# Performance work log

Measured on AMD Instinct MI355X. Metric: run time of the kernel, lower is better.

## Reference

```python
import jax, jax.numpy as jnp
import numpy as np
from functools import partial

K = 64
KERNEL_SIZE = 16
TAU = 10.0
THETA = 0.5
GAMMA = 10.0
ALPHA = float(np.exp(-1.0 / TAU))
BETA = 1.0 - ALPHA

@jax.custom_vjp
def spike(x):
    return (x >= 0).astype(x.dtype)

def _spike_fwd(x):
    return spike(x), x

def _spike_bwd(x, g):
    surrogate = GAMMA * jnp.maximum(1.0 - GAMMA * jnp.abs(x), 0.0)
    return (g * surrogate,)

spike.defvjp(_spike_fwd, _spike_bwd)

def setup_inputs() -> dict:
    key = jax.random.key(0)
    k1, k2 = jax.random.split(key)
    B, T = 256, 4096
    x = jax.random.normal(k1, (B, 1, T), dtype=jnp.float32)
    # conv weight [K, 1, ks], init N(0, 1/sqrt(ks))
    W = jax.random.normal(k2, (K, 1, KERNEL_SIZE), dtype=jnp.float32) / np.sqrt(KERNEL_SIZE)
    return {"x": x, "W": W}

def _forward(x, W):
    B = x.shape[0]
    x = x.reshape(B, 1, -1)  # [B,1,T]
    # causal conv: left pad ks-1 -> output length T
    u = jax.lax.conv_general_dilated(
        x, W,
        window_strides=(1,),
        padding=[(KERNEL_SIZE - 1, 0)],
        dimension_numbers=("NCH", "OIH", "NCH"),
    )  # [B,K,T]
    u_t = jnp.transpose(u, (2, 0, 1))  # [T,B,K]
    v0 = jnp.zeros((B, K), dtype=x.dtype)

    def step(v, ut):
        v = ALPHA * v + BETA * ut                      # leak + input
        s_raw = spike(v - THETA)                        # [B,K]
        winner = jax.lax.stop_gradient(jnp.argmax(v, axis=1))  # [B]
        winner_spiked = jnp.take_along_axis(s_raw, winner[:, None], axis=1)  # [B,1]
        wta_mask = jax.nn.one_hot(winner, K, dtype=s_raw.dtype) * winner_spiked
        s = s_raw * wta_mask
        v = v - s * THETA                               # reset
        return v, s

    _, spikes_t = jax.lax.scan(step, v0, u_t)  # [T,B,K]
    return jnp.transpose(spikes_t, (1, 2, 0))  # [B,K,T]

def reference(x, W):
    return _forward(x, W)
```

## Files before the change

kernel.cpp:

```cpp
#include <hip/hip_runtime.h>

#define T_LEN  4096
#define KS     16
#define NSEG   8
#define SEG_CH 32
#define WARM_CH 20
#define USTRIDE 18

#define ALPHA_F 0.9048374180359595f
#define BETA_F  0.09516258196404048f
#define THETA_F 0.5f

__device__ __forceinline__ void barrier_lds() {
  asm volatile("s_waitcnt lgkmcnt(0)\n\ts_barrier" ::: "memory");
}

__device__ __forceinline__ float wave64_max_all(float v) {
  float m, t;
  asm("s_nop 1\n\t"
      "v_max_f32 %0, %2, %2 quad_perm:[1,0,3,2] row_mask:0xf bank_mask:0xf\n\t"
      "s_nop 1\n\t"
      "v_max_f32 %0, %0, %0 quad_perm:[2,3,0,1] row_mask:0xf bank_mask:0xf\n\t"
      "s_nop 1\n\t"
      "v_max_f32 %0, %0, %0 row_half_mirror row_mask:0xf bank_mask:0xf\n\t"
      "s_nop 1\n\t"
      "v_max_f32 %0, %0, %0 row_mirror row_mask:0xf bank_mask:0xf\n\t"
      "v_mov_b32 %1, %0\n\t"
      "s_nop 1\n\t"
      "v_permlane32_swap_b32 %1, %0\n\t"
      "s_nop 1\n\t"
      "v_max_f32 %0, %0, %1\n\t"
      "v_mov_b32 %1, %0\n\t"
      "s_nop 1\n\t"
      "v_permlane16_swap_b32 %1, %0\n\t"
      "s_nop 1\n\t"
      "v_max_f32 %0, %0, %1"
      : "=&v"(m), "=&v"(t)
      : "v"(v));
  return m;
}

__global__ __launch_bounds__(128, 4)
void convlif_wta_kernel(const float* __restrict__ x, const float* __restrict__ W,
                        float* __restrict__ out) {
  const int blk  = blockIdx.x;
  const int b    = blk >> 3;
  const int seg  = blk & (NSEG - 1);
  const int wave = threadIdx.x >> 6;
  const int lane = threadIdx.x & 63;

  const int cout0  = seg * SEG_CH;
  const int cstart = (cout0 > WARM_CH) ? (cout0 - WARM_CH) : 0;
  const int cend   = cout0 + SEG_CH;
  const int wpairs = (cout0 - cstart) >> 1;
  const int npair  = (cend - cstart) >> 1;

  __shared__ float dbuf[2][2][64][USTRIDE];

  const float4* xv4 = reinterpret_cast<const float4*>(x + (size_t)b * T_LEN);
  float* orow = out + ((size_t)(b * 64 + lane)) * T_LEN;

  if (wave == 1) {
    float w[KS];
    {
      const float4* w4 = reinterpret_cast<const float4*>(W + lane * KS);
      #pragma unroll
      for (int q = 0; q < 4; ++q) {
        float4 a = w4[q];
        w[4*q+0] = a.x; w[4*q+1] = a.y; w[4*q+2] = a.z; w[4*q+3] = a.w;
      }
    }

    for (int p = 0; p < npair; ++p) {
      #pragma unroll
      for (int ch = 0; ch < 2; ++ch) {
        const int c = cstart + 2 * p + ch;
        float xf[32];
        if (c == 0) {
          #pragma unroll
          for (int m = 0; m < 16; ++m) xf[m] = 0.0f;
        } else {
          const int b4 = 4 * c - 4;
          #pragma unroll
          for (int q = 0; q < 4; ++q) {
            float4 a = xv4[b4 + q];
            xf[4*q+0] = a.x; xf[4*q+1] = a.y; xf[4*q+2] = a.z; xf[4*q+3] = a.w;
          }
        }
        #pragma unroll
        for (int q = 0; q < 4; ++q) {
          float4 a = xv4[4*c + q];
          xf[16+4*q+0] = a.x; xf[16+4*q+1] = a.y;
          xf[16+4*q+2] = a.z; xf[16+4*q+3] = a.w;
        }

        float* ur = &dbuf[p & 1][ch][lane][0];
        #pragma unroll
        for (int i = 0; i < 16; i += 2) {
          float acc0 = w[0] * xf[1 + i];
          #pragma unroll
          for (int j = 1; j < KS; ++j) acc0 = fmaf(w[j], xf[1 + i + j], acc0);
          float acc1 = w[0] * xf[2 + i];
          #pragma unroll
          for (int j = 1; j < KS; ++j) acc1 = fmaf(w[j], xf[2 + i + j], acc1);
          *reinterpret_cast<float2*>(ur + i) =
              make_float2(BETA_F * acc0, BETA_F * acc1);
        }
      }
      barrier_lds();
    }
    barrier_lds();
  } else {
    float v = 0.0f;

    barrier_lds();

    for (int q = 0; q < wpairs; ++q) {
      const int slot = q & 1;
      #pragma unroll
      for (int ch = 0; ch < 2; ++ch) {
        float u[16];
        {
          const float* ur = &dbuf[slot][ch][lane][0];
          #pragma unroll
          for (int i = 0; i < 16; i += 2) {
            float2 t2 = *reinterpret_cast<const float2*>(ur + i);
            u[i] = t2.x; u[i + 1] = t2.y;
          }
        }
        #pragma unroll
        for (int i = 0; i < 16; ++i) {
          float vr = fmaf(ALPHA_F, v, u[i]);
          float vm = vr - THETA_F;
          unsigned long long sp = __ballot(vr >= THETA_F);
          bool c1 = (vr >= THETA_F);
          v = c1 ? vm : vr;
          if (__builtin_expect((sp & (sp - 1ull)) != 0ull, 0)) {
            float m = wave64_max_all(vr);
            unsigned long long eq = __ballot(vr == m);
            bool win = (lane == __builtin_ctzll(eq));
            v = win ? vm : vr;
          }
        }
      }
      barrier_lds();
    }

    for (int q = wpairs; q < npair; ++q) {
      const int slot = q & 1;
      #pragma unroll
      for (int ch = 0; ch < 2; ++ch) {
        const int c = cstart + 2 * q + ch;
        float u[16];
        {
          const float* ur = &dbuf[slot][ch][lane][0];
          #pragma unroll
          for (int i = 0; i < 16; i += 2) {
            float2 t2 = *reinterpret_cast<const float2*>(ur + i);
            u[i] = t2.x; u[i + 1] = t2.y;
          }
        }
        float sv[16];
        #pragma unroll
        for (int i = 0; i < 16; ++i) {
          float vr = fmaf(ALPHA_F, v, u[i]);
          float vm = vr - THETA_F;
          unsigned long long sp = __ballot(vr >= THETA_F);
          bool c1 = (vr >= THETA_F);
          sv[i] = c1 ? 1.0f : 0.0f;
          v     = c1 ? vm : vr;
          if (__builtin_expect((sp & (sp - 1ull)) != 0ull, 0)) {
            float m = wave64_max_all(vr);
            unsigned long long eq = __ballot(vr == m);
            bool win = (lane == __builtin_ctzll(eq));
            sv[i] = win ? 1.0f : 0.0f;
            v     = win ? vm : vr;
          }
        }
        float4* pp = reinterpret_cast<float4*>(orow + (size_t)c * 16);
        pp[0] = make_float4(sv[0],  sv[1],  sv[2],  sv[3]);
        pp[1] = make_float4(sv[4],  sv[5],  sv[6],  sv[7]);
        pp[2] = make_float4(sv[8],  sv[9],  sv[10], sv[11]);
        pp[3] = make_float4(sv[12], sv[13], sv[14], sv[15]);
      }
      barrier_lds();
    }
  }
}

extern "C" void kernel_launch(void* const* d_in, const int* in_sizes, int n_in,
                              void* d_out, int out_size, void* d_ws, size_t ws_size,
                              hipStream_t stream) {
  const float* x   = (const float*)d_in[0];
  const float* W   = (const float*)d_in[1];
  float*       out = (float*)d_out;
  convlif_wta_kernel<<<dim3(256 * NSEG), dim3(128), 0, stream>>>(x, W, out);
}
```

Before: 105.9 us.

## Split conv work between producer and consumer waves to balance load

The producer wave now computes the first 16 timesteps of the first chunk and only 8 of the second chunk in each pair. The consumer wave loads x directly and computes the remaining 8 conv outputs itself, before running the scan. This is meant to cut the producer's per-pair conv time, which gates the barrier pipeline, by moving part of its work onto the scan wave. In exchange the consumer wave takes extra global loads and FMAs, and every wave now loads the weights.

```diff
diff --git a/kernel.cpp b/kernel.cpp
--- a/kernel.cpp
+++ b/kernel.cpp
@@ -60,27 +60,28 @@
   const float4* xv4 = reinterpret_cast<const float4*>(x + (size_t)b * T_LEN);
   float* orow = out + ((size_t)(b * 64 + lane)) * T_LEN;
 
+  float w[KS];
+  {
+    const float4* w4 = reinterpret_cast<const float4*>(W + lane * KS);
+    #pragma unroll
+    for (int q = 0; q < 4; ++q) {
+      float4 a = w4[q];
+      w[4*q+0] = a.x; w[4*q+1] = a.y; w[4*q+2] = a.z; w[4*q+3] = a.w;
+    }
+  }
+
   if (wave == 1) {
-    float w[KS];
-    {
-      const float4* w4 = reinterpret_cast<const float4*>(W + lane * KS);
-      #pragma unroll
-      for (int q = 0; q < 4; ++q) {
-        float4 a = w4[q];
-        w[4*q+0] = a.x; w[4*q+1] = a.y; w[4*q+2] = a.z; w[4*q+3] = a.w;
-      }
-    }
-
     for (int p = 0; p < npair; ++p) {
-      #pragma unroll
-      for (int ch = 0; ch < 2; ++ch) {
-        const int c = cstart + 2 * p + ch;
+      const int c0 = cstart + 2 * p;
+      const int c1 = c0 + 1;
+
+      {
         float xf[32];
-        if (c == 0) {
+        if (c0 == 0) {
           #pragma unroll
           for (int m = 0; m < 16; ++m) xf[m] = 0.0f;
         } else {
-          const int b4 = 4 * c - 4;
+          const int b4 = 4 * c0 - 4;
           #pragma unroll
           for (int q = 0; q < 4; ++q) {
             float4 a = xv4[b4 + q];
@@ -89,14 +90,35 @@
         }
         #pragma unroll
         for (int q = 0; q < 4; ++q) {
-          float4 a = xv4[4*c + q];
+          float4 a = xv4[4*c0 + q];
           xf[16+4*q+0] = a.x; xf[16+4*q+1] = a.y;
           xf[16+4*q+2] = a.z; xf[16+4*q+3] = a.w;
         }
-
-        float* ur = &dbuf[p & 1][ch][lane][0];
+        float* ur = &dbuf[p & 1][0][lane][0];
         #pragma unroll
         for (int i = 0; i < 16; i += 2) {
+          float acc0 = w[0] * xf[1 + i];
+          #pragma unroll
+          for (int j = 1; j < KS; ++j) acc0 = fmaf(w[j], xf[1 + i + j], acc0);
+          float acc1 = w[0] * xf[2 + i];
+          #pragma unroll
+          for (int j = 1; j < KS; ++j) acc1 = fmaf(w[j], xf[2 + i + j], acc1);
+          *reinterpret_cast<float2*>(ur + i) =
+              make_float2(BETA_F * acc0, BETA_F * acc1);
+        }
+      }
+
+      {
+        float xf[24];
+        const int b4 = 4 * c1 - 4;
+        #pragma unroll
+        for (int q = 0; q < 6; ++q) {
+          float4 a = xv4[b4 + q];
+          xf[4*q+0] = a.x; xf[4*q+1] = a.y; xf[4*q+2] = a.z; xf[4*q+3] = a.w;
+        }
+        float* ur = &dbuf[p & 1][1][lane][0];
+        #pragma unroll
+        for (int i = 0; i < 8; i += 2) {
           float acc0 = w[0] * xf[1 + i];
           #pragma unroll
           for (int j = 1; j < KS; ++j) acc0 = fmaf(w[j], xf[1 + i + j], acc0);
@@ -112,63 +134,59 @@
     barrier_lds();
   } else {
     float v = 0.0f;
-
     barrier_lds();
 
-    for (int q = 0; q < wpairs; ++q) {
+    for (int q = 0; q < npair; ++q) {
       const int slot = q & 1;
+      const int c0 = cstart + 2 * q;
+      const int c1 = c0 + 1;
+      const bool outp = (q >= wpairs);
+
+      float u0[16], u1lo[8];
+      {
+        const float* ur0 = &dbuf[slot][0][lane][0];
+        #pragma unroll
+        for (int i = 0; i < 16; i += 2) {
+          float2 t2 = *reinterpret_cast<const float2*>(ur0 + i);
+          u0[i] = t2.x; u0[i + 1] = t2.y;
+        }
+        const float* ur1 = &dbuf[slot][1][lane][0];
+        #pragma unroll
+        for (int i = 0; i < 8; i += 2) {
+          float2 t2 = *reinterpret_cast<const float2*>(ur1 + i);
+          u1lo[i] = t2.x; u1lo[i + 1] = t2.y;
+        }
+      }
+
+      float xh[24];
+      {
+        const int bq = 4 * c1 - 2;
+        #pragma unroll
+        for (int qq = 0; qq < 6; ++qq) {
+          float4 a = xv4[bq + qq];
+          xh[4*qq+0] = a.x; xh[4*qq+1] = a.y; xh[4*qq+2] = a.z; xh[4*qq+3] = a.w;
+        }
+      }
+
+      float uhi[8];
       #pragma unroll
-      for (int ch = 0; ch < 2; ++ch) {
-        float u[16];
-        {
-          const float* ur = &dbuf[slot][ch][lane][0];
-          #pragma unroll
-          for (int i = 0; i < 16; i += 2) {
-            float2 t2 = *reinterpret_cast<const float2*>(ur + i);
-            u[i] = t2.x; u[i + 1] = t2.y;
-          }
-        }
-        #pragma unroll
-        for (int i = 0; i < 16; ++i) {
-          float vr = fmaf(ALPHA_F, v, u[i]);
-          float vm = vr - THETA_F;
-          unsigned long long sp = __ballot(vr >= THETA_F);
-          bool c1 = (vr >= THETA_F);
-          v = c1 ? vm : vr;
-          if (__builtin_expect((sp & (sp - 1ull)) != 0ull, 0)) {
-            float m = wave64_max_all(vr);
-            unsigned long long eq = __ballot(vr == m);
-            bool win = (lane == __builtin_ctzll(eq));
-            v = win ? vm : vr;
-          }
-        }
-      }
-      barrier_lds();
-    }
-
-    for (int q = wpairs; q < npair; ++q) {
-      const int slot = q & 1;
-      #pragma unroll
-      for (int ch = 0; ch < 2; ++ch) {
-        const int c = cstart + 2 * q + ch;
-        float u[16];
-        {
-          const float* ur = &dbuf[slot][ch][lane][0];
-          #pragma unroll
-          for (int i = 0; i < 16; i += 2) {
-            float2 t2 = *reinterpret_cast<const float2*>(ur + i);
-            u[i] = t2.x; u[i + 1] = t2.y;
-          }
-        }
+      for (int i = 8; i < 16; ++i) {
+        float acc = w[0] * xh[i - 7];
+        #pragma unroll
+        for (int j = 1; j < KS; ++j) acc = fmaf(w[j], xh[i - 7 + j], acc);
+        uhi[i - 8] = BETA_F * acc;
+      }
+
+      if (outp) {
         float sv[16];
         #pragma unroll
         for (int i = 0; i < 16; ++i) {
-          float vr = fmaf(ALPHA_F, v, u[i]);
-          float vm = vr - THETA_F;
-          unsigned long long sp = __ballot(vr >= THETA_F);
-          bool c1 = (vr >= THETA_F);
-          sv[i] = c1 ? 1.0f : 0.0f;
-          v     = c1 ? vm : vr;
+          float vr = fmaf(ALPHA_F, v, u0[i]);
+          float vm = vr - THETA_F;
+          unsigned long long sp = __ballot(vr >= THETA_F);
+          bool c1b = (vr >= THETA_F);
+          sv[i] = c1b ? 1.0f : 0.0f;
+          v     = c1b ? vm : vr;
           if (__builtin_expect((sp & (sp - 1ull)) != 0ull, 0)) {
             float m = wave64_max_all(vr);
             unsigned long long eq = __ballot(vr == m);
@@ -177,12 +195,70 @@
             v     = win ? vm : vr;
           }
         }
-        float4* pp = reinterpret_cast<float4*>(orow + (size_t)c * 16);
+        float4* pp = reinterpret_cast<float4*>(orow + (size_t)c0 * 16);
         pp[0] = make_float4(sv[0],  sv[1],  sv[2],  sv[3]);
         pp[1] = make_float4(sv[4],  sv[5],  sv[6],  sv[7]);
         pp[2] = make_float4(sv[8],  sv[9],  sv[10], sv[11]);
         pp[3] = make_float4(sv[12], sv[13], sv[14], sv[15]);
-      }
+      } else {
+        #pragma unroll
+        for (int i = 0; i < 16; ++i) {
+          float vr = fmaf(ALPHA_F, v, u0[i]);
+          float vm = vr - THETA_F;
+          unsigned long long sp = __ballot(vr >= THETA_F);
+          bool c1b = (vr >= THETA_F);
+          v = c1b ? vm : vr;
+          if (__builtin_expect((sp & (sp - 1ull)) != 0ull, 0)) {
+            float m = wave64_max_all(vr);
+            unsigned long long eq = __ballot(vr == m);
+            bool win = (lane == __builtin_ctzll(eq));
+            v = win ? vm : vr;
+          }
+        }
+      }
+
+      if (outp) {
+        float sv[16];
+        #pragma unroll
+        for (int i = 0; i < 16; ++i) {
+          float ui = (i < 8) ? u1lo[i] : uhi[i - 8];
+          float vr = fmaf(ALPHA_F, v, ui);
+          float vm = vr - THETA_F;
+          unsigned long long sp = __ballot(vr >= THETA_F);
+          bool c1b = (vr >= THETA_F);
+          sv[i] = c1b ? 1.0f : 0.0f;
+          v     = c1b ? vm : vr;
+          if (__builtin_expect((sp & (sp - 1ull)) != 0ull, 0)) {
+            float m = wave64_max_all(vr);
+            unsigned long long eq = __ballot(vr == m);
+            bool win = (lane == __builtin_ctzll(eq));
+            sv[i] = win ? 1.0f : 0.0f;
+            v     = win ? vm : vr;
+          }
+        }
+        float4* pp = reinterpret_cast<float4*>(orow + (size_t)c1 * 16);
+        pp[0] = make_float4(sv[0],  sv[1],  sv[2],  sv[3]);
+        pp[1] = make_float4(sv[4],  sv[5],  sv[6],  sv[7]);
+        pp[2] = make_float4(sv[8],  sv[9],  sv[10], sv[11]);
+        pp[3] = make_float4(sv[12], sv[13], sv[14], sv[15]);
+      } else {
+        #pragma unroll
+        for (int i = 0; i < 16; ++i) {
+          float ui = (i < 8) ? u1lo[i] : uhi[i - 8];
+          float vr = fmaf(ALPHA_F, v, ui);
+          float vm = vr - THETA_F;
+          unsigned long long sp = __ballot(vr >= THETA_F);
+          bool c1b = (vr >= THETA_F);
+          v = c1b ? vm : vr;
+          if (__builtin_expect((sp & (sp - 1ull)) != 0ull, 0)) {
+            float m = wave64_max_all(vr);
+            unsigned long long eq = __ballot(vr == m);
+            bool win = (lane == __builtin_ctzll(eq));
+            v = win ? vm : vr;
+          }
+        }
+      }
+
       barrier_lds();
     }
   }
```

New measurement: 110.5 us. 1.04x slower.
